# Kernel tuning notes

Hardware: AMD Instinct MI355X
Metric: run time of the kernel (lower is better)

## Reference

```python
import jax, jax.numpy as jnp
import numpy as np

N, M, E = 100000, 500, 300000
XS, GS, OUT, HEADS = 100, 100, 100, 2
SLOPE = 0.2
EPS = 1e-12


def l2norm(x, axis):
    n = jnp.linalg.norm(x, axis=axis, keepdims=True)
    return x / jnp.maximum(n, EPS)


def gat_layer(h_ijk, ends, n, W, att):
    # W: [heads*out, in_dim] (no bias); att: [1, heads, out]
    heads, out = att.shape[1], att.shape[2]
    c = (h_ijk @ W.T).reshape(-1, heads, out)               # [E, H, D]
    a = jnp.sum(att * c, axis=2, keepdims=True)             # [E, H, 1]
    e = jnp.exp(-jax.nn.leaky_relu(a, SLOPE))
    denom = jax.ops.segment_sum(e, ends, num_segments=n)    # [n, H, 1]
    alpha = e / denom[ends]                                 # segment softmax (dropout=eval/identity)
    h = jax.ops.segment_sum(alpha * c, ends, num_segments=n)  # [n, H, D]
    h = jax.nn.elu(h)
    h = l2norm(h, axis=2)
    return h.reshape(n, heads * out)


def merge_layer(h_in, h_out, Wi, bi, Wo, bo, Wl, bl):
    hi = h_in @ Wi.T + bi
    ho = h_out @ Wo.T + bo
    lam = jax.nn.sigmoid(jnp.concatenate([hi, ho], axis=1) @ Wl.T + bl)
    h = lam * hi + (1.0 - lam) * ho
    return l2norm(jax.nn.elu(h), axis=1)


def setup_inputs() -> dict:
    key = jax.random.key(0)
    ks = jax.random.split(key, 24)
    D = HEADS * OUT  # 200
    in1 = 2 * XS + GS   # 300
    in2 = 3 * D         # 600
    s = 0.05
    return {
        'edge_idx': jax.random.randint(ks[0], (2, E), 0, N),
        'edge_type': jax.random.randint(ks[1], (E,), 0, M),
        'path_idx': jax.random.randint(ks[2], (2, 8), 0, N),
        'path_type': jax.random.randint(ks[3], (2, 8), 0, M),
        'use_path': 0,
        'x': jax.random.normal(ks[4], (N, XS), jnp.float32),
        'g': jax.random.normal(ks[5], (M, GS), jnp.float32),
        'W_in1': s * jax.random.normal(ks[6], (D, in1), jnp.float32),
        'att_in1': s * jax.random.normal(ks[7], (1, HEADS, OUT), jnp.float32),
        'W_out1': s * jax.random.normal(ks[8], (D, in1), jnp.float32),
        'att_out1': s * jax.random.normal(ks[9], (1, HEADS, OUT), jnp.float32),
        'Wi1': s * jax.random.normal(ks[10], (D, D), jnp.float32), 'bi1': jnp.zeros((D,), jnp.float32),
        'Wo1': s * jax.random.normal(ks[11], (D, D), jnp.float32), 'bo1': jnp.zeros((D,), jnp.float32),
        'Wl1': s * jax.random.normal(ks[12], (1, 2 * D), jnp.float32), 'bl1': jnp.zeros((1,), jnp.float32),
        'Wr': s * jax.random.normal(ks[13], (D, GS), jnp.float32), 'br': jnp.zeros((D,), jnp.float32),
        'Wf': s * jax.random.normal(ks[14], (D, in1), jnp.float32), 'bf': jnp.zeros((D,), jnp.float32),
        'W_in2': s * jax.random.normal(ks[15], (D, in2), jnp.float32),
        'att_in2': s * jax.random.normal(ks[16], (1, 1, D), jnp.float32),
        'W_out2': s * jax.random.normal(ks[17], (D, in2), jnp.float32),
        'att_out2': s * jax.random.normal(ks[18], (1, 1, D), jnp.float32),
        'Wi2': s * jax.random.normal(ks[19], (D, D), jnp.float32), 'bi2': jnp.zeros((D,), jnp.float32),
        'Wo2': s * jax.random.normal(ks[20], (D, D), jnp.float32), 'bo2': jnp.zeros((D,), jnp.float32),
        'Wl2': s * jax.random.normal(ks[21], (1, 2 * D), jnp.float32), 'bl2': jnp.zeros((1,), jnp.float32),
        'W_ent': s * jax.random.normal(ks[22], (D, XS), jnp.float32),
    }


def reference(edge_idx, edge_type, path_idx, path_type, use_path, x, g,
              W_in1, att_in1, W_out1, att_out1, Wi1, bi1, Wo1, bo1, Wl1, bl1,
              Wr, br, Wf, bf,
              W_in2, att_in2, W_out2, att_out2, Wi2, bi2, Wo2, bo2, Wl2, bl2,
              W_ent):
    n, m = x.shape[0], g.shape[0]
    x = l2norm(x, axis=1)  # x_initial is renormalized each forward
    row, col = edge_idx[0], edge_idx[1]
    # hop 1: gather-concat per-edge features [E, 2*XS+GS]
    h_ijk = jnp.concatenate([x[row], x[col], g[edge_type]], axis=1)
    h_in = gat_layer(h_ijk, col, n, W_in1, att_in1)
    h_out = gat_layer(h_ijk, row, n, W_out1, att_out1)
    h = merge_layer(h_in, h_out, Wi1, bi1, Wo1, bo1, Wl1, bl1)
    # relation layer
    g_edges = jax.ops.segment_sum(h_ijk, edge_type, num_segments=m)
    g_edges = jax.nn.elu(l2norm(g_edges, axis=1))
    g_prime = (g @ Wr.T + br) + (g_edges @ Wf.T + bf)
    # hop 2
    h_ijk2 = jnp.concatenate([h[row], h[col], g_prime[edge_type]], axis=1)
    h_in2 = gat_layer(h_ijk2, col, n, W_in2, att_in2)
    h_out2 = gat_layer(h_ijk2, row, n, W_out2, att_out2)
    h = merge_layer(h_in2, h_out2, Wi2, bi2, Wo2, bo2, Wl2, bl2)
    # entity residual layer
    h_prime = x @ W_ent.T + h
    return h_prime
```

## Files before the change

kernel.cpp:

```cpp
#include <hip/hip_runtime.h>
#include <cstddef>
#include <cstdint>

#define WSLOPE 0.2f
#define WEPS 1e-12f

typedef __attribute__((ext_vector_type(8))) short bf16x8;
typedef __attribute__((ext_vector_type(4))) float f32x4;

__device__ __forceinline__ float waveSum(float v) {
#pragma unroll
    for (int off = 32; off > 0; off >>= 1) v += __shfl_xor(v, off, 64);
    return v;
}
__device__ __forceinline__ float eluf(float v) { return v > 0.f ? v : expm1f(v); }
__device__ __forceinline__ short f2bf(float f) {
    union { float f; uint32_t u; } v; v.f = f;
    uint32_t r = v.u + 0x7FFF + ((v.u >> 16) & 1);
    return (short)(r >> 16);
}
__device__ __forceinline__ float bf2f(short s) {
    union { uint32_t u; float f; } v; v.u = ((uint32_t)(uint16_t)s) << 16;
    return v.f;
}

__global__ void k_invnorm(const float* __restrict__ x, float* __restrict__ invn, int N) {
    int wid = blockIdx.x * 4 + (threadIdx.x >> 6);
    int lane = threadIdx.x & 63;
    if (wid >= N) return;
    const float* p = x + (size_t)wid * 100;
    float a = p[lane];
    float ss = a * a;
    if (lane < 36) { float b = p[lane + 64]; ss += b * b; }
    ss = waveSum(ss);
    if (lane == 0) invn[wid] = 1.f / fmaxf(sqrtf(ss), WEPS);
}

__global__ void k_count(const int* __restrict__ keys, int* __restrict__ cnt, int n) {
    int i = blockIdx.x * 256 + threadIdx.x;
    if (i < n) atomicAdd(&cnt[keys[i]], 1);
}

#define SCAN_CHUNK 2048
__global__ void k_blocksum(const int* __restrict__ cnt, int* __restrict__ bsum, int n) {
    __shared__ int sh[256];
    int b = blockIdx.x, t = threadIdx.x;
    int base = b * SCAN_CHUNK;
    int s = 0;
    for (int i = t; i < SCAN_CHUNK; i += 256) { int idx = base + i; if (idx < n) s += cnt[idx]; }
    sh[t] = s; __syncthreads();
    for (int off = 128; off > 0; off >>= 1) { if (t < off) sh[t] += sh[t + off]; __syncthreads(); }
    if (t == 0) bsum[b] = sh[0];
}

__global__ void k_scanwrite(const int* __restrict__ cnt, const int* __restrict__ bsum,
                            int* __restrict__ offs, int* __restrict__ cur, int n, int nb) {
    __shared__ int sh[256];
    __shared__ int sbase;
    int b = blockIdx.x, t = threadIdx.x;
    if (t == 0) { int s = 0; for (int i = 0; i < b; ++i) s += bsum[i]; sbase = s; }
    __syncthreads();
    int base = b * SCAN_CHUNK;
    int loc[8]; int ts = 0;
#pragma unroll
    for (int i = 0; i < 8; ++i) { int idx = base + t * 8 + i; int v = (idx < n) ? cnt[idx] : 0; loc[i] = ts; ts += v; }
    sh[t] = ts; __syncthreads();
    for (int off = 1; off < 256; off <<= 1) {
        int v = (t >= off) ? sh[t - off] : 0;
        __syncthreads();
        sh[t] += v;
        __syncthreads();
    }
    int excl = (t == 0) ? 0 : sh[t - 1];
    int gbase = sbase + excl;
#pragma unroll
    for (int i = 0; i < 8; ++i) {
        int idx = base + t * 8 + i;
        if (idx < n) { offs[idx] = gbase + loc[i]; cur[idx] = gbase + loc[i]; }
    }
    if (b == nb - 1 && t == 255) offs[n] = sbase + sh[255];
}

__global__ void k_scatter3(const int* __restrict__ keys, const int* __restrict__ other,
                           const int* __restrict__ et, int* __restrict__ cur,
                           int* __restrict__ nbrS, int* __restrict__ etS,
                           int* __restrict__ keyS, int n) {
    int i = blockIdx.x * 256 + threadIdx.x;
    if (i < n) {
        int p = atomicAdd(&cur[keys[i]], 1);
        nbrS[p] = other[i];
        etS[p] = et[i];
        keyS[p] = keys[i];
    }
}

__global__ void k_scatter2(const int* __restrict__ keys, int* __restrict__ cur,
                           int* __restrict__ rs, int* __restrict__ cs,
                           const int* __restrict__ row, const int* __restrict__ col, int n) {
    int i = blockIdx.x * 256 + threadIdx.x;
    if (i < n) {
        int p = atomicAdd(&cur[keys[i]], 1);
        rs[p] = row[i];
        cs[p] = col[i];
    }
}

__global__ void k_watt(const float* __restrict__ att, const float* __restrict__ W,
                       float* __restrict__ wa, int H, int DH, int K) {
    int id = blockIdx.x * 256 + threadIdx.x;
    if (id >= H * K) return;
    int h = id / K, k = id % K;
    float s = 0.f;
    for (int j = 0; j < DH; ++j) s += att[h * DH + j] * W[(size_t)(h * DH + j) * K + k];
    wa[id] = s;
}

template<bool HOP2>
__global__ void k_dots(const float* __restrict__ feat, const float* __restrict__ invn,
                       const float* __restrict__ wa, float* __restrict__ rdot,
                       float* __restrict__ cdot, int N) {
    int wid = blockIdx.x * 4 + (threadIdx.x >> 6);
    int lane = threadIdx.x & 63;
    if (wid >= N) return;
    if (!HOP2) {
        float inv = invn[wid];
        const float* p = feat + (size_t)wid * 100;
        float f0 = p[lane] * inv;
        float f1 = (lane < 36) ? p[lane + 64] * inv : 0.f;
#pragma unroll
        for (int h = 0; h < 2; ++h) {
            const float* w = wa + h * 300;
            float r = f0 * w[lane] + ((lane < 36) ? f1 * w[lane + 64] : 0.f);
            float c = f0 * w[100 + lane] + ((lane < 36) ? f1 * w[100 + lane + 64] : 0.f);
            r = waveSum(r); c = waveSum(c);
            if (lane == 0) { rdot[wid * 2 + h] = r; cdot[wid * 2 + h] = c; }
        }
    } else {
        const float* p = feat + (size_t)wid * 200;
        float r = 0.f, c = 0.f;
#pragma unroll
        for (int m = 0; m < 4; ++m) {
            int d = lane + m * 64;
            if (d < 200) { float f = p[d]; r += f * wa[d]; c += f * wa[200 + d]; }
        }
        r = waveSum(r); c = waveSum(c);
        if (lane == 0) { rdot[wid] = r; cdot[wid] = c; }
    }
}

__global__ void k_gdot(const float* __restrict__ gsrc, const float* __restrict__ wa,
                       float* __restrict__ gdot, int M, int H, int GL, int K) {
    int id = blockIdx.x * 256 + threadIdx.x;
    if (id >= M * H) return;
    int m = id / H, h = id % H;
    float s = 0.f;
    const float* w = wa + h * K + 2 * GL;
    const float* gm = gsrc + (size_t)m * GL;
    for (int kk = 0; kk < GL; ++kk) s += gm[kk] * w[kk];
    gdot[id] = s;
}

__global__ void k_ew_s(const int* __restrict__ nbrS, const int* __restrict__ keyS,
                       const int* __restrict__ etS,
                       const float* __restrict__ ndot, const float* __restrict__ kdot,
                       const float* __restrict__ gdot, float* __restrict__ ewS, int E, int H) {
    int id = blockIdx.x * 256 + threadIdx.x;
    if (id >= E * H) return;
    int p = id / H, h = id - p * H;
    float a = ndot[nbrS[p] * H + h] + kdot[keyS[p] * H + h] + gdot[etS[p] * H + h];
    float lr = a > 0.f ? a : WSLOPE * a;
    ewS[id] = expf(-lr);
}

template<bool HOP2>
__global__ void k_agg(const int* __restrict__ offs, const int* __restrict__ nbrS,
                      const int* __restrict__ etS, const float* __restrict__ ewS,
                      const short* __restrict__ featB, const short* __restrict__ gB,
                      short* __restrict__ A, int n0, int n1) {
    constexpr int H = HOP2 ? 1 : 2;
    constexpr int LDA = HOP2 ? 672 : 576;
    constexpr int FW = HOP2 ? 224 : 112;
    constexpr int GW = HOP2 ? 224 : 112;
    int node = n0 + blockIdx.x * 4 + (threadIdx.x >> 6);
    int lane = threadIdx.x & 63;
    if (node >= n1) return;
    int o = offs[node];
    int deg = offs[node + 1] - o;
    float va[7];
#pragma unroll
    for (int m = 0; m < 7; ++m) va[m] = 0.f;
    if (deg > 0) {
        float s0 = 0.f, s1 = 0.f;
        for (int i = lane; i < deg; i += 64) {
            s0 += ewS[(size_t)(o + i) * H];
            if (H == 2) s1 += ewS[(size_t)(o + i) * H + 1];
        }
        s0 = waveSum(s0);
        float rd0 = 1.f / s0, rd1 = rd0;
        if (H == 2) { s1 = waveSum(s1); rd1 = 1.f / s1; }
        for (int j = 0; j < deg; ++j) {
            float a0 = ewS[(size_t)(o + j) * H] * rd0;
            float a1 = (H == 2) ? ewS[(size_t)(o + j) * H + 1] * rd1 : a0;
            int nbr = nbrS[o + j];
            int et = etS[o + j];
            const short* fr = featB + (size_t)nbr * FW;
            const short* gr = gB + (size_t)et * GW;
            if (!HOP2) {
#pragma unroll
                for (int m = 0; m < 7; ++m) {
                    int d = lane + m * 64;
                    if (d < 100) va[m] += a0 * bf2f(fr[d]);
                    else if (d < 200) va[m] += a1 * bf2f(fr[d - 100]);
                    else if (d < 300) va[m] += a0 * bf2f(gr[d - 200]);
                    else if (d < 400) va[m] += a1 * bf2f(gr[d - 300]);
                }
            } else {
#pragma unroll
                for (int m = 0; m < 7; ++m) {
                    int d = lane + m * 64;
                    if (d < 200) va[m] += a0 * bf2f(fr[d]);
                    else if (d < 424) va[m] += a0 * bf2f(gr[d - 200]);
                }
            }
        }
    }
    size_t rb = (size_t)(node - n0);
    short* Ar = A + rb * LDA;
    if (!HOP2) {
#pragma unroll
        for (int m = 0; m < 7; ++m) {
            int d = lane + m * 64;
            if (d < 400) {
                int col = d < 100 ? d : (d < 200 ? d + 12 : (d < 300 ? d + 24 : d + 36));
                Ar[col] = f2bf(va[m]);
            }
        }
        if (lane < 48) { int q = lane / 12; int rm = lane - q * 12; Ar[q * 112 + 100 + rm] = 0; }
        const short* sf = featB + (size_t)node * 112;
#pragma unroll
        for (int mm = 0; mm < 2; ++mm) {
            int k = lane + mm * 64;
            if (k < 128) Ar[448 + k] = (deg > 0 && k < 112) ? sf[k] : (short)0;
        }
    } else {
#pragma unroll
        for (int m = 0; m < 7; ++m) {
            int d = lane + m * 64;
            if (d < 424) Ar[d < 200 ? d : d + 24] = f2bf(va[m]);
        }
        if (lane < 24) Ar[200 + lane] = 0;
        const short* sf = featB + (size_t)node * 224;
#pragma unroll
        for (int mm = 0; mm < 4; ++mm) {
            int k = lane + mm * 64;
            if (k < 224) Ar[448 + k] = deg > 0 ? sf[k] : (short)0;
        }
    }
}

template<int KSTEPS, bool BIAS, bool ACC>
__launch_bounds__(256)
__global__ void k_mgemm(const short* __restrict__ A, const short* __restrict__ Wb,
                        const float* __restrict__ bias,
                        float* __restrict__ out, int rows, int lda) {
    constexpr int LDW = KSTEPS * 32;
    const int t = threadIdx.x;
    const int wv = t >> 6, l = t & 63;
    const int lhi = l >> 4, llo = l & 15;
    const int rbase = blockIdx.x * 64 + wv * 16;
    f32x4 acc[13];
#pragma unroll
    for (int j = 0; j < 13; ++j) acc[j] = f32x4{0.f, 0.f, 0.f, 0.f};
    const short* arow = A + (size_t)(rbase + llo) * lda + lhi * 8;
#pragma unroll
    for (int kt = 0; kt < KSTEPS; ++kt) {
        bf16x8 a = *(const bf16x8*)(arow + kt * 32);
#pragma unroll
        for (int j = 0; j < 13; ++j) {
            bf16x8 b = *(const bf16x8*)(Wb + (size_t)(j * 16 + llo) * LDW + kt * 32 + lhi * 8);
            acc[j] = __builtin_amdgcn_mfma_f32_16x16x32_bf16(a, b, acc[j], 0, 0, 0);
        }
    }
    const int r0 = rbase + lhi * 4;
#pragma unroll
    for (int e = 0; e < 4; ++e) {
        int r = r0 + e;
        if (r >= rows) continue;
        float* orow = out + (size_t)r * 200;
#pragma unroll
        for (int j = 0; j < 13; ++j) {
            int d = j * 16 + llo;
            if (d < 200) {
                float v = acc[j][e];
                if (BIAS) v += bias[d];
                if (ACC) v += orow[d];
                orow[d] = v;
            }
        }
    }
}

__global__ void k_prepw(const float* __restrict__ W, int ldW, int koff, int Klen, int span,
                        int mode, short* __restrict__ Wb, int ldWb, int dst) {
    int id = blockIdx.x * 256 + threadIdx.x;
    int tot = 208 * span;
    if (id >= tot) return;
    int d = id / span, k = id - d * span;
    float v = 0.f;
    if (d < 200) {
        if (mode == 0) { if (k < Klen) v = W[(size_t)d * ldW + koff + k]; }
        else { int h = d / 100; int kk = k - h * 112; if (kk >= 0 && kk < Klen) v = W[(size_t)d * ldW + koff + kk]; }
    }
    Wb[(size_t)d * ldWb + dst + k] = f2bf(v);
}

__global__ void k_prepwrf(const float* __restrict__ Wr, const float* __restrict__ Wf,
                          short* __restrict__ Wb) {
    int id = blockIdx.x * 256 + threadIdx.x;
    if (id >= 208 * 448) return;
    int d = id / 448, k = id - d * 448;
    float v = 0.f;
    if (d < 200) {
        if (k < 100) v = Wr[(size_t)d * 100 + k];
        else if (k >= 128 && k < 428) v = Wf[(size_t)d * 300 + (k - 128)];
    }
    Wb[id] = f2bf(v);
}

__global__ void k_brf(const float* __restrict__ br, const float* __restrict__ bf,
                      float* __restrict__ brf) {
    int d = threadIdx.x;
    if (d < 200) brf[d] = br[d] + bf[d];
}

__global__ void k_cvt112(const float* __restrict__ src, const float* __restrict__ invn,
                         short* __restrict__ dst, int rows) {
    int id = blockIdx.x * 256 + threadIdx.x;
    if (id >= rows * 112) return;
    int r = id / 112, k = id - r * 112;
    float v = 0.f;
    if (k < 100) { v = src[(size_t)r * 100 + k]; if (invn) v *= invn[r]; }
    dst[id] = f2bf(v);
}

__global__ void k_gcb(const float* __restrict__ g, short* __restrict__ gb, int rows) {
    int id = blockIdx.x * 256 + threadIdx.x;
    if (id >= rows * 128) return;
    int r = id >> 7, k = id & 127;
    gb[(size_t)r * 448 + k] = f2bf(k < 100 ? g[(size_t)r * 100 + k] : 0.f);
}

__global__ void k_h1b(const float* __restrict__ h1, short* __restrict__ sb, int rows) {
    int id = blockIdx.x * 256 + threadIdx.x;
    if (id >= rows * 224) return;
    int r = id / 224, k = id - r * 224;
    sb[id] = f2bf(k < 200 ? h1[(size_t)r * 200 + k] : 0.f);
}

template<int DH, int H>
__global__ void gat_post2(const float* __restrict__ hb, short* __restrict__ pb, int rowsH) {
    int nh = blockIdx.x * 4 + (threadIdx.x >> 6);
    int lane = threadIdx.x & 63;
    if (nh >= rowsH) return;
    const float* p = hb + (size_t)nh * DH;
    constexpr int MM = (DH + 63) / 64;
    float v[MM];
    float ss = 0.f;
#pragma unroll
    for (int m = 0; m < MM; ++m) {
        int d = lane + m * 64;
        v[m] = 0.f;
        if (d < DH) { v[m] = eluf(p[d]); ss += v[m] * v[m]; }
    }
    ss = waveSum(ss);
    float inv = 1.f / fmaxf(sqrtf(ss), WEPS);
    short* ob = pb + (size_t)(nh / H) * 224 + (size_t)(nh % H) * DH;
#pragma unroll
    for (int m = 0; m < MM; ++m) {
        int d = lane + m * 64;
        if (d < DH) ob[d] = f2bf(v[m] * inv);
    }
}

__global__ void merge_comb(const float* __restrict__ hi, const float* __restrict__ ho,
                           const float* __restrict__ Wl, const float* __restrict__ bl,
                           float* __restrict__ out, short* __restrict__ hbf, int N) {
    int wid = blockIdx.x * 4 + (threadIdx.x >> 6);
    int lane = threadIdx.x & 63;
    if (wid >= N) return;
    float vi[4], vo[4];
    float s = 0.f;
#pragma unroll
    for (int m = 0; m < 4; ++m) {
        int d = lane + m * 64;
        vi[m] = 0.f; vo[m] = 0.f;
        if (d < 200) {
            vi[m] = hi[(size_t)wid * 200 + d];
            vo[m] = ho[(size_t)wid * 200 + d];
            s += Wl[d] * vi[m] + Wl[200 + d] * vo[m];
        }
    }
    s = waveSum(s);
    float lam = 1.f / (1.f + expf(-(s + bl[0])));
    float hv[4];
    float ss = 0.f;
#pragma unroll
    for (int m = 0; m < 4; ++m) {
        int d = lane + m * 64;
        hv[m] = 0.f;
        if (d < 200) {
            float h = lam * vi[m] + (1.f - lam) * vo[m];
            hv[m] = eluf(h);
            ss += hv[m] * hv[m];
        }
    }
    ss = waveSum(ss);
    float inv = 1.f / fmaxf(sqrtf(ss), WEPS);
#pragma unroll
    for (int m = 0; m < 4; ++m) {
        int d = lane + m * 64;
        if (d < 200) {
            float v = hv[m] * inv;
            out[(size_t)wid * 200 + d] = v;
            if (hbf) hbf[(size_t)wid * 224 + d] = f2bf(v);
        } else if (d < 224) {
            if (hbf) hbf[(size_t)wid * 224 + d] = 0;
        }
    }
}

__global__ void k_gedges_b(const int* __restrict__ rsT, const int* __restrict__ csT,
                           const int* __restrict__ offsT,
                           const float* __restrict__ x, const float* __restrict__ invn,
                           const float* __restrict__ g, short* __restrict__ gcomb, int M) {
    __shared__ float red[6];
    int m = blockIdx.x, t = threadIdx.x;
    int o = offsT[m];
    int deg = offsT[m + 1] - o;
    float acc = 0.f;
    if (t < 128) {
        int d = t; bool ok = d < 100;
        for (int i = 0; i < deg; ++i) {
            int r = rsT[o + i];
            if (ok) acc += x[(size_t)r * 100 + d] * invn[r];
        }
    } else if (t < 256) {
        int d = t - 128; bool ok = d < 100;
        for (int i = 0; i < deg; ++i) {
            int c = csT[o + i];
            if (ok) acc += x[(size_t)c * 100 + d] * invn[c];
        }
    } else {
        int d = t - 256;
        if (d < 100) acc = (float)deg * g[(size_t)m * 100 + d];
    }
    float sq = waveSum(acc * acc);
    if ((t & 63) == 0) red[t >> 6] = sq;
    __syncthreads();
    float s2 = red[0] + red[1] + red[2] + red[3] + red[4] + red[5];
    float inv = 1.f / fmaxf(sqrtf(s2), WEPS);
    short* orow = gcomb + (size_t)m * 448 + 128;
    if (t < 128) {
        if (t < 100) orow[t] = f2bf(eluf(acc * inv));
    } else if (t < 256) {
        int d = t - 128;
        if (d < 100) orow[100 + d] = f2bf(eluf(acc * inv));
    } else {
        int d = t - 256;
        if (d < 100) orow[200 + d] = f2bf(eluf(acc * inv));
        else if (d < 120) orow[200 + d] = 0;
    }
}

extern "C" void kernel_launch(void* const* d_in, const int* in_sizes, int n_in,
                              void* d_out, int out_size, void* d_ws, size_t ws_size,
                              hipStream_t stream) {
    const int* eidx   = (const int*)d_in[0];
    const int* etype  = (const int*)d_in[1];
    const float* x    = (const float*)d_in[5];
    const float* g    = (const float*)d_in[6];
    const float* W_in1  = (const float*)d_in[7];
    const float* att_in1 = (const float*)d_in[8];
    const float* W_out1 = (const float*)d_in[9];
    const float* att_out1 = (const float*)d_in[10];
    const float* Wi1 = (const float*)d_in[11]; const float* bi1 = (const float*)d_in[12];
    const float* Wo1 = (const float*)d_in[13]; const float* bo1 = (const float*)d_in[14];
    const float* Wl1 = (const float*)d_in[15]; const float* bl1 = (const float*)d_in[16];
    const float* Wr  = (const float*)d_in[17]; const float* br  = (const float*)d_in[18];
    const float* Wf  = (const float*)d_in[19]; const float* bf  = (const float*)d_in[20];
    const float* W_in2  = (const float*)d_in[21]; const float* att_in2 = (const float*)d_in[22];
    const float* W_out2 = (const float*)d_in[23]; const float* att_out2 = (const float*)d_in[24];
    const float* Wi2 = (const float*)d_in[25]; const float* bi2 = (const float*)d_in[26];
    const float* Wo2 = (const float*)d_in[27]; const float* bo2 = (const float*)d_in[28];
    const float* Wl2 = (const float*)d_in[29]; const float* bl2 = (const float*)d_in[30];
    const float* W_ent = (const float*)d_in[31];

    const int E = in_sizes[1];
    const int N = in_sizes[5] / 100;
    const int M = in_sizes[6] / 100;
    const int Mr = (M + 63) & ~63;
    float* out = (float*)d_out;
    const int* row = eidx;
    const int* col = eidx + E;

    char* w = (char*)d_ws;
    size_t off_b = 0;
    auto alloc = [&](size_t bytes) -> void* {
        void* p = w + off_b;
        off_b += (bytes + 255) & ~(size_t)255;
        return p;
    };
    float* invn  = (float*)alloc((size_t)N * 4);
    float* h1    = (float*)alloc((size_t)N * 200 * 4);
    short* h1_bf = (short*)alloc((size_t)(N + 64) * 224 * 2);
    short* xn_bf = (short*)alloc((size_t)(N + 64) * 112 * 2);
    short* g_bf  = (short*)alloc((size_t)M * 112 * 2);
    int* offs_in = (int*)alloc((size_t)(N + 1) * 4);
    int* offs_out= (int*)alloc((size_t)(N + 1) * 4);
    int* offsT   = (int*)alloc((size_t)(M + 1) * 4);
    int* nbrS_in = (int*)alloc((size_t)E * 4);
    int* etS_in  = (int*)alloc((size_t)E * 4);
    int* keyS_in = (int*)alloc((size_t)E * 4);
    int* nbrS_out= (int*)alloc((size_t)E * 4);
    int* etS_out = (int*)alloc((size_t)E * 4);
    int* keyS_out= (int*)alloc((size_t)E * 4);
    int* rsT     = (int*)alloc((size_t)E * 4);
    int* csT     = (int*)alloc((size_t)E * 4);
    int* cnt     = (int*)alloc((size_t)N * 4);
    int* cur     = (int*)alloc((size_t)N * 4);
    int* bsum    = (int*)alloc((size_t)64 * 4);
    float* wa_in = (float*)alloc((size_t)1200 * 4);
    float* wa_out= (float*)alloc((size_t)1200 * 4);
    float* rdot_in = (float*)alloc((size_t)N * 2 * 4);
    float* cdot_in = (float*)alloc((size_t)N * 2 * 4);
    float* rdot_out= (float*)alloc((size_t)N * 2 * 4);
    float* cdot_out= (float*)alloc((size_t)N * 2 * 4);
    float* gdot_in = (float*)alloc((size_t)M * 2 * 4);
    float* gdot_out= (float*)alloc((size_t)M * 2 * 4);
    float* ewS_in  = (float*)alloc((size_t)E * 2 * 4);
    float* ewS_out = (float*)alloc((size_t)E * 2 * 4);
    float* gp      = (float*)alloc((size_t)M * 200 * 4);
    short* gcomb   = (short*)alloc((size_t)Mr * 448 * 2);
    short* Wc_in1  = (short*)alloc((size_t)208 * 576 * 2);
    short* Wc_out1 = (short*)alloc((size_t)208 * 576 * 2);
    short* Wc_in2  = (short*)alloc((size_t)208 * 672 * 2);
    short* Wc_out2 = (short*)alloc((size_t)208 * 672 * 2);
    short* Wm_i1   = (short*)alloc((size_t)208 * 224 * 2);
    short* Wm_o1   = (short*)alloc((size_t)208 * 224 * 2);
    short* Wm_i2   = (short*)alloc((size_t)208 * 224 * 2);
    short* Wm_o2   = (short*)alloc((size_t)208 * 224 * 2);
    short* Wb_ent  = (short*)alloc((size_t)208 * 128 * 2);
    short* Wrf_b   = (short*)alloc((size_t)208 * 448 * 2);
    float* brf     = (float*)alloc((size_t)200 * 4);

    if (off_b >= ws_size) return;
    size_t rem = ws_size - off_b;
    long long Cll = (long long)(rem / 3520);
    long long Nr64 = ((long long)N + 63) & ~63LL;
    int C = (int)(Cll > Nr64 ? Nr64 : Cll);
    C &= ~63;
    if (C < 64) return;
    float* hbA   = (float*)alloc((size_t)C * 200 * 4);
    float* hbB   = (float*)alloc((size_t)C * 200 * 4);
    short* Ac    = (short*)alloc((size_t)C * 672 * 2);
    short* post_b= (short*)alloc((size_t)C * 224 * 2);
    if (off_b > ws_size) return;

    const int gE = (E + 255) / 256;
    const int gN4 = (N + 3) / 4;
    const int gM64 = (M + 63) / 64;

    k_invnorm<<<gN4, 256, 0, stream>>>(x, invn, N);

    hipMemsetAsync(post_b, 0, (size_t)C * 224 * 2, stream);

    k_cvt112<<<((int)(((size_t)N * 112 + 255) / 256)), 256, 0, stream>>>(x, invn, xn_bf, N);
    k_cvt112<<<((int)(((size_t)M * 112 + 255) / 256)), 256, 0, stream>>>(g, nullptr, g_bf, M);

    auto gsp = [](int span) { return (208 * span + 255) / 256; };
    k_prepw<<<gsp(224), 256, 0, stream>>>(W_in1, 300, 0, 100, 224, 1, Wc_in1, 576, 0);
    k_prepw<<<gsp(224), 256, 0, stream>>>(W_in1, 300, 200, 100, 224, 1, Wc_in1, 576, 224);
    k_prepw<<<gsp(128), 256, 0, stream>>>(W_in1, 300, 100, 100, 128, 0, Wc_in1, 576, 448);
    k_prepw<<<gsp(224), 256, 0, stream>>>(W_out1, 300, 100, 100, 224, 1, Wc_out1, 576, 0);
    k_prepw<<<gsp(224), 256, 0, stream>>>(W_out1, 300, 200, 100, 224, 1, Wc_out1, 576, 224);
    k_prepw<<<gsp(128), 256, 0, stream>>>(W_out1, 300, 0, 100, 128, 0, Wc_out1, 576, 448);
    k_prepw<<<gsp(224), 256, 0, stream>>>(W_in2, 600, 0, 200, 224, 0, Wc_in2, 672, 0);
    k_prepw<<<gsp(224), 256, 0, stream>>>(W_in2, 600, 400, 200, 224, 0, Wc_in2, 672, 224);
    k_prepw<<<gsp(224), 256, 0, stream>>>(W_in2, 600, 200, 200, 224, 0, Wc_in2, 672, 448);
    k_prepw<<<gsp(224), 256, 0, stream>>>(W_out2, 600, 200, 200, 224, 0, Wc_out2, 672, 0);
    k_prepw<<<gsp(224), 256, 0, stream>>>(W_out2, 600, 400, 200, 224, 0, Wc_out2, 672, 224);
    k_prepw<<<gsp(224), 256, 0, stream>>>(W_out2, 600, 0, 200, 224, 0, Wc_out2, 672, 448);
    k_prepw<<<gsp(224), 256, 0, stream>>>(Wi1, 200, 0, 200, 224, 0, Wm_i1, 224, 0);
    k_prepw<<<gsp(224), 256, 0, stream>>>(Wo1, 200, 0, 200, 224, 0, Wm_o1, 224, 0);
    k_prepw<<<gsp(224), 256, 0, stream>>>(Wi2, 200, 0, 200, 224, 0, Wm_i2, 224, 0);
    k_prepw<<<gsp(224), 256, 0, stream>>>(Wo2, 200, 0, 200, 224, 0, Wm_o2, 224, 0);
    k_prepw<<<gsp(128), 256, 0, stream>>>(W_ent, 100, 0, 100, 128, 0, Wb_ent, 128, 0);
    k_prepwrf<<<gsp(448), 256, 0, stream>>>(Wr, Wf, Wrf_b);
    k_brf<<<1, 256, 0, stream>>>(br, bf, brf);

    int nbN = (N + SCAN_CHUNK - 1) / SCAN_CHUNK;
    int nbM = (M + SCAN_CHUNK - 1) / SCAN_CHUNK;
    hipMemsetAsync(cnt, 0, (size_t)N * 4, stream);
    k_count<<<gE, 256, 0, stream>>>(col, cnt, E);
    k_blocksum<<<nbN, 256, 0, stream>>>(cnt, bsum, N);
    k_scanwrite<<<nbN, 256, 0, stream>>>(cnt, bsum, offs_in, cur, N, nbN);
    k_scatter3<<<gE, 256, 0, stream>>>(col, row, etype, cur, nbrS_in, etS_in, keyS_in, E);

    hipMemsetAsync(cnt, 0, (size_t)N * 4, stream);
    k_count<<<gE, 256, 0, stream>>>(row, cnt, E);
    k_blocksum<<<nbN, 256, 0, stream>>>(cnt, bsum, N);
    k_scanwrite<<<nbN, 256, 0, stream>>>(cnt, bsum, offs_out, cur, N, nbN);
    k_scatter3<<<gE, 256, 0, stream>>>(row, col, etype, cur, nbrS_out, etS_out, keyS_out, E);

    hipMemsetAsync(cnt, 0, (size_t)M * 4, stream);
    k_count<<<gE, 256, 0, stream>>>(etype, cnt, E);
    k_blocksum<<<nbM, 256, 0, stream>>>(cnt, bsum, M);
    k_scanwrite<<<nbM, 256, 0, stream>>>(cnt, bsum, offsT, cur, M, nbM);
    k_scatter2<<<gE, 256, 0, stream>>>(etype, cur, rsT, csT, row, col, E);

    k_watt<<<(2 * 300 + 255) / 256, 256, 0, stream>>>(att_in1, W_in1, wa_in, 2, 100, 300);
    k_watt<<<(2 * 300 + 255) / 256, 256, 0, stream>>>(att_out1, W_out1, wa_out, 2, 100, 300);
    k_dots<false><<<gN4, 256, 0, stream>>>(x, invn, wa_in, rdot_in, cdot_in, N);
    k_dots<false><<<gN4, 256, 0, stream>>>(x, invn, wa_out, rdot_out, cdot_out, N);
    k_gdot<<<(M * 2 + 255) / 256, 256, 0, stream>>>(g, wa_in, gdot_in, M, 2, 100, 300);
    k_gdot<<<(M * 2 + 255) / 256, 256, 0, stream>>>(g, wa_out, gdot_out, M, 2, 100, 300);
    k_ew_s<<<(E * 2 + 255) / 256, 256, 0, stream>>>(nbrS_in, keyS_in, etS_in, rdot_in, cdot_in, gdot_in, ewS_in, E, 2);
    k_ew_s<<<(E * 2 + 255) / 256, 256, 0, stream>>>(nbrS_out, keyS_out, etS_out, cdot_out, rdot_out, gdot_out, ewS_out, E, 2);
    k_gcb<<<((int)(((size_t)M * 128 + 255) / 256)), 256, 0, stream>>>(g, gcomb, M);

    for (int n0 = 0; n0 < N; n0 += C) {
        int rows = (N - n0 < C) ? (N - n0) : C;
        int n1 = n0 + rows;
        int ga = (rows + 3) / 4;
        int gb = (rows + 63) / 64;
        k_agg<false><<<ga, 256, 0, stream>>>(offs_in, nbrS_in, etS_in, ewS_in, xn_bf, g_bf, Ac, n0, n1);
        k_mgemm<18, false, false><<<gb, 256, 0, stream>>>(Ac, Wc_in1, nullptr, hbA, rows, 576);
        gat_post2<100, 2><<<(2 * rows + 3) / 4, 256, 0, stream>>>(hbA, post_b, 2 * rows);
        k_mgemm<7, true, false><<<gb, 256, 0, stream>>>(post_b, Wm_i1, bi1, hbA, rows, 224);
        k_agg<false><<<ga, 256, 0, stream>>>(offs_out, nbrS_out, etS_out, ewS_out, xn_bf, g_bf, Ac, n0, n1);
        k_mgemm<18, false, false><<<gb, 256, 0, stream>>>(Ac, Wc_out1, nullptr, hbB, rows, 576);
        gat_post2<100, 2><<<(2 * rows + 3) / 4, 256, 0, stream>>>(hbB, post_b, 2 * rows);
        k_mgemm<7, true, false><<<gb, 256, 0, stream>>>(post_b, Wm_o1, bo1, hbB, rows, 224);
        merge_comb<<<ga, 256, 0, stream>>>(hbA, hbB, Wl1, bl1, h1 + (size_t)n0 * 200,
                                           h1_bf + (size_t)n0 * 224, rows);
    }

    k_gedges_b<<<M, 384, 0, stream>>>(rsT, csT, offsT, x, invn, g, gcomb, M);
    k_mgemm<14, true, false><<<gM64, 256, 0, stream>>>(gcomb, Wrf_b, brf, gp, M, 448);

    k_watt<<<(600 + 255) / 256, 256, 0, stream>>>(att_in2, W_in2, wa_in, 1, 200, 600);
    k_watt<<<(600 + 255) / 256, 256, 0, stream>>>(att_out2, W_out2, wa_out, 1, 200, 600);
    k_dots<true><<<gN4, 256, 0, stream>>>(h1, nullptr, wa_in, rdot_in, cdot_in, N);
    k_dots<true><<<gN4, 256, 0, stream>>>(h1, nullptr, wa_out, rdot_out, cdot_out, N);
    k_gdot<<<(M + 255) / 256, 256, 0, stream>>>(gp, wa_in, gdot_in, M, 1, 200, 600);
    k_gdot<<<(M + 255) / 256, 256, 0, stream>>>(gp, wa_out, gdot_out, M, 1, 200, 600);
    k_h1b<<<((int)(((size_t)M * 224 + 255) / 256)), 256, 0, stream>>>(gp, gcomb, M);
    k_ew_s<<<(E + 255) / 256, 256, 0, stream>>>(nbrS_in, keyS_in, etS_in, rdot_in, cdot_in, gdot_in, ewS_in, E, 1);
    k_ew_s<<<(E + 255) / 256, 256, 0, stream>>>(nbrS_out, keyS_out, etS_out, cdot_out, rdot_out, gdot_out, ewS_out, E, 1);

    for (int n0 = 0; n0 < N; n0 += C) {
        int rows = (N - n0 < C) ? (N - n0) : C;
        int n1 = n0 + rows;
        int ga = (rows + 3) / 4;
        int gb = (rows + 63) / 64;
        k_agg<true><<<ga, 256, 0, stream>>>(offs_in, nbrS_in, etS_in, ewS_in, h1_bf, gcomb, Ac, n0, n1);
        k_mgemm<21, false, false><<<gb, 256, 0, stream>>>(Ac, Wc_in2, nullptr, hbA, rows, 672);
        gat_post2<200, 1><<<ga, 256, 0, stream>>>(hbA, post_b, rows);
        k_mgemm<7, true, false><<<gb, 256, 0, stream>>>(post_b, Wm_i2, bi2, hbA, rows, 224);
        k_agg<true><<<ga, 256, 0, stream>>>(offs_out, nbrS_out, etS_out, ewS_out, h1_bf, gcomb, Ac, n0, n1);
        k_mgemm<21, false, false><<<gb, 256, 0, stream>>>(Ac, Wc_out2, nullptr, hbB, rows, 672);
        gat_post2<200, 1><<<ga, 256, 0, stream>>>(hbB, post_b, rows);
        k_mgemm<7, true, false><<<gb, 256, 0, stream>>>(post_b, Wm_o2, bo2, hbB, rows, 224);
        merge_comb<<<ga, 256, 0, stream>>>(hbA, hbB, Wl2, bl2, out + (size_t)n0 * 200, nullptr, rows);
        k_mgemm<4, false, true><<<gb, 256, 0, stream>>>(xn_bf + (size_t)n0 * 112, Wb_ent, nullptr,
                                                        out + (size_t)n0 * 200, rows, 112);
    }
}
```

Before: 2.887 ms.

## Fuse GAT epilogues, merge layer and hop-2 attention dots into MFMA GEMM kernels

The ELU+L2-norm post-processing now runs in the GEMM epilogue, and the two merge projections plus the sigmoid gate, ELU and norm run in one dual-GEMM kernel. Hop-2 attention dot products come from that same epilogue, and relation-layer g' dots come from its GEMM epilogue. This drops the fp32 intermediate buffers (h1, hbA/hbB, gp), several separate launches and the kernels that reread those buffers. It frees workspace for larger chunks, at the cost of higher register pressure in the fused kernels and 16-lane shuffle reductions.

```diff
diff --git a/kernel.cpp b/kernel.cpp
--- a/kernel.cpp
+++ b/kernel.cpp
@@ -11,6 +11,11 @@
 __device__ __forceinline__ float waveSum(float v) {
 #pragma unroll
     for (int off = 32; off > 0; off >>= 1) v += __shfl_xor(v, off, 64);
+    return v;
+}
+__device__ __forceinline__ float rowSum16(float v) {
+#pragma unroll
+    for (int off = 8; off > 0; off >>= 1) v += __shfl_xor(v, off, 64);
     return v;
 }
 __device__ __forceinline__ float eluf(float v) { return v > 0.f ? v : expm1f(v); }
@@ -115,49 +120,44 @@
     wa[id] = s;
 }
 
-template<bool HOP2>
-__global__ void k_dots(const float* __restrict__ feat, const float* __restrict__ invn,
-                       const float* __restrict__ wa, float* __restrict__ rdot,
-                       float* __restrict__ cdot, int N) {
+__global__ void k_dots2(const float* __restrict__ x, const float* __restrict__ invn,
+                        const float* __restrict__ wai, const float* __restrict__ wao,
+                        float* __restrict__ rdi, float* __restrict__ cdi,
+                        float* __restrict__ rdo, float* __restrict__ cdo, int N) {
     int wid = blockIdx.x * 4 + (threadIdx.x >> 6);
     int lane = threadIdx.x & 63;
     if (wid >= N) return;
-    if (!HOP2) {
-        float inv = invn[wid];
-        const float* p = feat + (size_t)wid * 100;
-        float f0 = p[lane] * inv;
-        float f1 = (lane < 36) ? p[lane + 64] * inv : 0.f;
-#pragma unroll
-        for (int h = 0; h < 2; ++h) {
-            const float* w = wa + h * 300;
-            float r = f0 * w[lane] + ((lane < 36) ? f1 * w[lane + 64] : 0.f);
-            float c = f0 * w[100 + lane] + ((lane < 36) ? f1 * w[100 + lane + 64] : 0.f);
-            r = waveSum(r); c = waveSum(c);
-            if (lane == 0) { rdot[wid * 2 + h] = r; cdot[wid * 2 + h] = c; }
-        }
-    } else {
-        const float* p = feat + (size_t)wid * 200;
-        float r = 0.f, c = 0.f;
-#pragma unroll
-        for (int m = 0; m < 4; ++m) {
-            int d = lane + m * 64;
-            if (d < 200) { float f = p[d]; r += f * wa[d]; c += f * wa[200 + d]; }
-        }
-        r = waveSum(r); c = waveSum(c);
-        if (lane == 0) { rdot[wid] = r; cdot[wid] = c; }
-    }
-}
-
-__global__ void k_gdot(const float* __restrict__ gsrc, const float* __restrict__ wa,
-                       float* __restrict__ gdot, int M, int H, int GL, int K) {
-    int id = blockIdx.x * 256 + threadIdx.x;
-    if (id >= M * H) return;
-    int m = id / H, h = id % H;
-    float s = 0.f;
-    const float* w = wa + h * K + 2 * GL;
-    const float* gm = gsrc + (size_t)m * GL;
-    for (int kk = 0; kk < GL; ++kk) s += gm[kk] * w[kk];
-    gdot[id] = s;
+    float inv = invn[wid];
+    const float* p = x + (size_t)wid * 100;
+    float f0 = p[lane] * inv;
+    float f1 = (lane < 36) ? p[lane + 64] * inv : 0.f;
+#pragma unroll
+    for (int h = 0; h < 2; ++h) {
+        const float* wi = wai + h * 300;
+        const float* wo = wao + h * 300;
+        float ri = f0 * wi[lane] + ((lane < 36) ? f1 * wi[lane + 64] : 0.f);
+        float ci = f0 * wi[100 + lane] + ((lane < 36) ? f1 * wi[100 + lane + 64] : 0.f);
+        float ro = f0 * wo[lane] + ((lane < 36) ? f1 * wo[lane + 64] : 0.f);
+        float co = f0 * wo[100 + lane] + ((lane < 36) ? f1 * wo[100 + lane + 64] : 0.f);
+        ri = waveSum(ri); ci = waveSum(ci); ro = waveSum(ro); co = waveSum(co);
+        if (lane == 0) { rdi[wid * 2 + h] = ri; cdi[wid * 2 + h] = ci; rdo[wid * 2 + h] = ro; cdo[wid * 2 + h] = co; }
+    }
+}
+
+__global__ void k_gdot4(const float* __restrict__ g, const float* __restrict__ wai,
+                        const float* __restrict__ wao, float* __restrict__ gdi,
+                        float* __restrict__ gdo, int M) {
+    int m = blockIdx.x * 256 + threadIdx.x;
+    if (m >= M) return;
+    const float* gm = g + (size_t)m * 100;
+    float s0 = 0.f, s1 = 0.f, s2 = 0.f, s3 = 0.f;
+    for (int k = 0; k < 100; ++k) {
+        float v = gm[k];
+        s0 += v * wai[200 + k]; s1 += v * wai[500 + k];
+        s2 += v * wao[200 + k]; s3 += v * wao[500 + k];
+    }
+    gdi[m * 2] = s0; gdi[m * 2 + 1] = s1;
+    gdo[m * 2] = s2; gdo[m * 2 + 1] = s3;
 }
 
 __global__ void k_ew_s(const int* __restrict__ nbrS, const int* __restrict__ keyS,
@@ -300,6 +300,191 @@
     }
 }
 
+template<int KSTEPS, int H>
+__launch_bounds__(256)
+__global__ void k_mgemm_post(const short* __restrict__ A, const short* __restrict__ Wb,
+                             short* __restrict__ post, int rows, int lda) {
+    constexpr int LDW = KSTEPS * 32;
+    const int t = threadIdx.x;
+    const int wv = t >> 6, l = t & 63;
+    const int lhi = l >> 4, llo = l & 15;
+    const int rbase = blockIdx.x * 64 + wv * 16;
+    f32x4 acc[13];
+#pragma unroll
+    for (int j = 0; j < 13; ++j) acc[j] = f32x4{0.f, 0.f, 0.f, 0.f};
+    const short* arow = A + (size_t)(rbase + llo) * lda + lhi * 8;
+#pragma unroll
+    for (int kt = 0; kt < KSTEPS; ++kt) {
+        bf16x8 a = *(const bf16x8*)(arow + kt * 32);
+#pragma unroll
+        for (int j = 0; j < 13; ++j) {
+            bf16x8 b = *(const bf16x8*)(Wb + (size_t)(j * 16 + llo) * LDW + kt * 32 + lhi * 8);
+            acc[j] = __builtin_amdgcn_mfma_f32_16x16x32_bf16(a, b, acc[j], 0, 0, 0);
+        }
+    }
+    const int r0 = rbase + lhi * 4;
+#pragma unroll
+    for (int e = 0; e < 4; ++e) {
+        int r = r0 + e;
+        if (r >= rows) continue;
+        float v[13];
+        float s0 = 0.f, s1 = 0.f;
+#pragma unroll
+        for (int j = 0; j < 13; ++j) {
+            int d = j * 16 + llo;
+            if (d < 200) {
+                float xv = eluf(acc[j][e]);
+                v[j] = xv;
+                if (H == 1 || d < 100) s0 += xv * xv; else s1 += xv * xv;
+            }
+        }
+        s0 = rowSum16(s0);
+        float inv0 = 1.f / fmaxf(sqrtf(s0), WEPS);
+        float inv1 = inv0;
+        if (H == 2) { s1 = rowSum16(s1); inv1 = 1.f / fmaxf(sqrtf(s1), WEPS); }
+        short* pr = post + (size_t)r * 224;
+#pragma unroll
+        for (int j = 0; j < 13; ++j) {
+            int d = j * 16 + llo;
+            if (d < 200) pr[d] = f2bf(v[j] * ((H == 2 && d >= 100) ? inv1 : inv0));
+        }
+    }
+}
+
+template<bool HOP1>
+__launch_bounds__(256)
+__global__ void k_mergemm(const short* __restrict__ pA, const short* __restrict__ pB,
+                          const short* __restrict__ Wi, const short* __restrict__ Wo,
+                          const float* __restrict__ bi, const float* __restrict__ bo,
+                          const float* __restrict__ Wl, const float* __restrict__ bl,
+                          float* __restrict__ outf, short* __restrict__ h1b,
+                          const float* __restrict__ wa2i, const float* __restrict__ wa2o,
+                          float* __restrict__ rdi, float* __restrict__ cdi,
+                          float* __restrict__ rdo, float* __restrict__ cdo,
+                          int rows) {
+    const int t = threadIdx.x;
+    const int wv = t >> 6, l = t & 63;
+    const int lhi = l >> 4, llo = l & 15;
+    const int rbase = blockIdx.x * 64 + wv * 16;
+    f32x4 accA[13], accB[13];
+#pragma unroll
+    for (int j = 0; j < 13; ++j) { accA[j] = f32x4{0.f, 0.f, 0.f, 0.f}; accB[j] = f32x4{0.f, 0.f, 0.f, 0.f}; }
+    const short* aA = pA + (size_t)(rbase + llo) * 224 + lhi * 8;
+    const short* aB = pB + (size_t)(rbase + llo) * 224 + lhi * 8;
+#pragma unroll
+    for (int kt = 0; kt < 7; ++kt) {
+        bf16x8 a1 = *(const bf16x8*)(aA + kt * 32);
+        bf16x8 a2 = *(const bf16x8*)(aB + kt * 32);
+#pragma unroll
+        for (int j = 0; j < 13; ++j) {
+            bf16x8 b1 = *(const bf16x8*)(Wi + (size_t)(j * 16 + llo) * 224 + kt * 32 + lhi * 8);
+            accA[j] = __builtin_amdgcn_mfma_f32_16x16x32_bf16(a1, b1, accA[j], 0, 0, 0);
+            bf16x8 b2 = *(const bf16x8*)(Wo + (size_t)(j * 16 + llo) * 224 + kt * 32 + lhi * 8);
+            accB[j] = __builtin_amdgcn_mfma_f32_16x16x32_bf16(a2, b2, accB[j], 0, 0, 0);
+        }
+    }
+    const int r0 = rbase + lhi * 4;
+    float blv = bl[0];
+#pragma unroll
+    for (int e = 0; e < 4; ++e) {
+        int r = r0 + e;
+        if (r >= rows) continue;
+        float vi[13], vo[13];
+        float lp = 0.f;
+#pragma unroll
+        for (int j = 0; j < 13; ++j) {
+            int d = j * 16 + llo;
+            if (d < 200) {
+                vi[j] = accA[j][e] + bi[d];
+                vo[j] = accB[j][e] + bo[d];
+                lp += Wl[d] * vi[j] + Wl[200 + d] * vo[j];
+            }
+        }
+        lp = rowSum16(lp);
+        float lam = 1.f / (1.f + expf(-(lp + blv)));
+        float hv[13];
+        float ss = 0.f;
+#pragma unroll
+        for (int j = 0; j < 13; ++j) {
+            int d = j * 16 + llo;
+            if (d < 200) { hv[j] = eluf(lam * vi[j] + (1.f - lam) * vo[j]); ss += hv[j] * hv[j]; }
+        }
+        ss = rowSum16(ss);
+        float inv = 1.f / fmaxf(sqrtf(ss), WEPS);
+        float ri = 0.f, ci = 0.f, ro = 0.f, co = 0.f;
+#pragma unroll
+        for (int j = 0; j < 13; ++j) {
+            int d = j * 16 + llo;
+            if (d < 200) {
+                float val = hv[j] * inv;
+                if (HOP1) {
+                    h1b[(size_t)r * 224 + d] = f2bf(val);
+                    ri += val * wa2i[d]; ci += val * wa2i[200 + d];
+                    ro += val * wa2o[d]; co += val * wa2o[200 + d];
+                } else {
+                    outf[(size_t)r * 200 + d] = val;
+                }
+            } else if (HOP1) {
+                h1b[(size_t)r * 224 + d] = 0;
+            }
+        }
+        if (HOP1) {
+            h1b[(size_t)r * 224 + 208 + llo] = 0;
+            ri = rowSum16(ri); ci = rowSum16(ci); ro = rowSum16(ro); co = rowSum16(co);
+            if (llo == 0) { rdi[r] = ri; cdi[r] = ci; rdo[r] = ro; cdo[r] = co; }
+        }
+    }
+}
+
+__launch_bounds__(256)
+__global__ void k_mgemm_rel(const short* __restrict__ A, const short* __restrict__ Wb,
+                            const float* __restrict__ brf,
+                            short* __restrict__ gout, const float* __restrict__ wai,
+                            const float* __restrict__ wao,
+                            float* __restrict__ gdi, float* __restrict__ gdo, int rows) {
+    constexpr int KSTEPS = 14, LDW = KSTEPS * 32;
+    const int t = threadIdx.x;
+    const int wv = t >> 6, l = t & 63;
+    const int lhi = l >> 4, llo = l & 15;
+    const int rbase = blockIdx.x * 64 + wv * 16;
+    f32x4 acc[13];
+#pragma unroll
+    for (int j = 0; j < 13; ++j) acc[j] = f32x4{0.f, 0.f, 0.f, 0.f};
+    const short* arow = A + (size_t)(rbase + llo) * 448 + lhi * 8;
+#pragma unroll
+    for (int kt = 0; kt < KSTEPS; ++kt) {
+        bf16x8 a = *(const bf16x8*)(arow + kt * 32);
+#pragma unroll
+        for (int j = 0; j < 13; ++j) {
+            bf16x8 b = *(const bf16x8*)(Wb + (size_t)(j * 16 + llo) * LDW + kt * 32 + lhi * 8);
+            acc[j] = __builtin_amdgcn_mfma_f32_16x16x32_bf16(a, b, acc[j], 0, 0, 0);
+        }
+    }
+    const int r0 = rbase + lhi * 4;
+#pragma unroll
+    for (int e = 0; e < 4; ++e) {
+        int r = r0 + e;
+        if (r >= rows) continue;
+        short* pr = gout + (size_t)r * 224;
+        float gi = 0.f, go = 0.f;
+#pragma unroll
+        for (int j = 0; j < 13; ++j) {
+            int d = j * 16 + llo;
+            if (d < 200) {
+                float val = acc[j][e] + brf[d];
+                pr[d] = f2bf(val);
+                gi += val * wai[400 + d];
+                go += val * wao[400 + d];
+            } else {
+                pr[d] = 0;
+            }
+        }
+        pr[208 + llo] = 0;
+        gi = rowSum16(gi); go = rowSum16(go);
+        if (llo == 0) { gdi[r] = gi; gdo[r] = go; }
+    }
+}
+
 __global__ void k_prepw(const float* __restrict__ W, int ldW, int koff, int Klen, int span,
                         int mode, short* __restrict__ Wb, int ldWb, int dst) {
     int id = blockIdx.x * 256 + threadIdx.x;
@@ -348,85 +533,6 @@
     if (id >= rows * 128) return;
     int r = id >> 7, k = id & 127;
     gb[(size_t)r * 448 + k] = f2bf(k < 100 ? g[(size_t)r * 100 + k] : 0.f);
-}
-
-__global__ void k_h1b(const float* __restrict__ h1, short* __restrict__ sb, int rows) {
-    int id = blockIdx.x * 256 + threadIdx.x;
-    if (id >= rows * 224) return;
-    int r = id / 224, k = id - r * 224;
-    sb[id] = f2bf(k < 200 ? h1[(size_t)r * 200 + k] : 0.f);
-}
-
-template<int DH, int H>
-__global__ void gat_post2(const float* __restrict__ hb, short* __restrict__ pb, int rowsH) {
-    int nh = blockIdx.x * 4 + (threadIdx.x >> 6);
-    int lane = threadIdx.x & 63;
-    if (nh >= rowsH) return;
-    const float* p = hb + (size_t)nh * DH;
-    constexpr int MM = (DH + 63) / 64;
-    float v[MM];
-    float ss = 0.f;
-#pragma unroll
-    for (int m = 0; m < MM; ++m) {
-        int d = lane + m * 64;
-        v[m] = 0.f;
-        if (d < DH) { v[m] = eluf(p[d]); ss += v[m] * v[m]; }
-    }
-    ss = waveSum(ss);
-    float inv = 1.f / fmaxf(sqrtf(ss), WEPS);
-    short* ob = pb + (size_t)(nh / H) * 224 + (size_t)(nh % H) * DH;
-#pragma unroll
-    for (int m = 0; m < MM; ++m) {
-        int d = lane + m * 64;
-        if (d < DH) ob[d] = f2bf(v[m] * inv);
-    }
-}
-
-__global__ void merge_comb(const float* __restrict__ hi, const float* __restrict__ ho,
-                           const float* __restrict__ Wl, const float* __restrict__ bl,
-                           float* __restrict__ out, short* __restrict__ hbf, int N) {
-    int wid = blockIdx.x * 4 + (threadIdx.x >> 6);
-    int lane = threadIdx.x & 63;
-    if (wid >= N) return;
-    float vi[4], vo[4];
-    float s = 0.f;
-#pragma unroll
-    for (int m = 0; m < 4; ++m) {
-        int d = lane + m * 64;
-        vi[m] = 0.f; vo[m] = 0.f;
-        if (d < 200) {
-            vi[m] = hi[(size_t)wid * 200 + d];
-            vo[m] = ho[(size_t)wid * 200 + d];
-            s += Wl[d] * vi[m] + Wl[200 + d] * vo[m];
-        }
-    }
-    s = waveSum(s);
-    float lam = 1.f / (1.f + expf(-(s + bl[0])));
-    float hv[4];
-    float ss = 0.f;
-#pragma unroll
-    for (int m = 0; m < 4; ++m) {
-        int d = lane + m * 64;
-        hv[m] = 0.f;
-        if (d < 200) {
-            float h = lam * vi[m] + (1.f - lam) * vo[m];
-            hv[m] = eluf(h);
-            ss += hv[m] * hv[m];
-        }
-    }
-    ss = waveSum(ss);
-    float inv = 1.f / fmaxf(sqrtf(ss), WEPS);
-#pragma unroll
-    for (int m = 0; m < 4; ++m) {
-        int d = lane + m * 64;
-        if (d < 200) {
-            float v = hv[m] * inv;
-            out[(size_t)wid * 200 + d] = v;
-            if (hbf) hbf[(size_t)wid * 224 + d] = f2bf(v);
-        } else if (d < 224) {
-            if (hbf) hbf[(size_t)wid * 224 + d] = 0;
-        }
-    }
 }
 
 __global__ void k_gedges_b(const int* __restrict__ rsT, const int* __restrict__ csT,
@@ -511,10 +617,10 @@
         return p;
     };
     float* invn  = (float*)alloc((size_t)N * 4);
-    float* h1    = (float*)alloc((size_t)N * 200 * 4);
     short* h1_bf = (short*)alloc((size_t)(N + 64) * 224 * 2);
     short* xn_bf = (short*)alloc((size_t)(N + 64) * 112 * 2);
     short* g_bf  = (short*)alloc((size_t)M * 112 * 2);
+    short* gp_bf = (short*)alloc((size_t)Mr * 224 * 2);
     int* offs_in = (int*)alloc((size_t)(N + 1) * 4);
     int* offs_out= (int*)alloc((size_t)(N + 1) * 4);
     int* offsT   = (int*)alloc((size_t)(M + 1) * 4);
@@ -529,8 +635,10 @@
     int* cnt     = (int*)alloc((size_t)N * 4);
     int* cur     = (int*)alloc((size_t)N * 4);
     int* bsum    = (int*)alloc((size_t)64 * 4);
-    float* wa_in = (float*)alloc((size_t)1200 * 4);
-    float* wa_out= (float*)alloc((size_t)1200 * 4);
+    float* wa1_in = (float*)alloc((size_t)640 * 4);
+    float* wa1_out= (float*)alloc((size_t)640 * 4);
+    float* wa2_in = (float*)alloc((size_t)640 * 4);
+    float* wa2_out= (float*)alloc((size_t)640 * 4);
     float* rdot_in = (float*)alloc((size_t)N * 2 * 4);
     float* cdot_in = (float*)alloc((size_t)N * 2 * 4);
     float* rdot_out= (float*)alloc((size_t)N * 2 * 4);
@@ -539,7 +647,6 @@
     float* gdot_out= (float*)alloc((size_t)M * 2 * 4);
     float* ewS_in  = (float*)alloc((size_t)E * 2 * 4);
     float* ewS_out = (float*)alloc((size_t)E * 2 * 4);
-    float* gp      = (float*)alloc((size_t)M * 200 * 4);
     short* gcomb   = (short*)alloc((size_t)Mr * 448 * 2);
     short* Wc_in1  = (short*)alloc((size_t)208 * 576 * 2);
     short* Wc_out1 = (short*)alloc((size_t)208 * 576 * 2);
@@ -555,15 +662,14 @@
 
     if (off_b >= ws_size) return;
     size_t rem = ws_size - off_b;
-    long long Cll = (long long)(rem / 3520);
+    long long Cll = (long long)(rem / 2368);
     long long Nr64 = ((long long)N + 63) & ~63LL;
     int C = (int)(Cll > Nr64 ? Nr64 : Cll);
     C &= ~63;
     if (C < 64) return;
-    float* hbA   = (float*)alloc((size_t)C * 200 * 4);
-    float* hbB   = (float*)alloc((size_t)C * 200 * 4);
     short* Ac    = (short*)alloc((size_t)C * 672 * 2);
-    short* post_b= (short*)alloc((size_t)C * 224 * 2);
+    short* postA = (short*)alloc((size_t)C * 224 * 2);
+    short* postB = (short*)alloc((size_t)C * 224 * 2);
     if (off_b > ws_size) return;
 
     const int gE = (E + 255) / 256;
@@ -572,7 +678,8 @@
 
     k_invnorm<<<gN4, 256, 0, stream>>>(x, invn, N);
 
-    hipMemsetAsync(post_b, 0, (size_t)C * 224 * 2, stream);
+    hipMemsetAsync(postA, 0, (size_t)C * 224 * 2, stream);
+    hipMemsetAsync(postB, 0, (size_t)C * 224 * 2, stream);
 
     k_cvt112<<<((int)(((size_t)N * 112 + 255) / 256)), 256, 0, stream>>>(x, invn, xn_bf, N);
     k_cvt112<<<((int)(((size_t)M * 112 + 255) / 256)), 256, 0, stream>>>(g, nullptr, g_bf, M);
@@ -618,12 +725,13 @@
     k_scanwrite<<<nbM, 256, 0, stream>>>(cnt, bsum, offsT, cur, M, nbM);
     k_scatter2<<<gE, 256, 0, stream>>>(etype, cur, rsT, csT, row, col, E);
 
-    k_watt<<<(2 * 300 + 255) / 256, 256, 0, stream>>>(att_in1, W_in1, wa_in, 2, 100, 300);
-    k_watt<<<(2 * 300 + 255) / 256, 256, 0, stream>>>(att_out1, W_out1, wa_out, 2, 100, 300);
-    k_dots<false><<<gN4, 256, 0, stream>>>(x, invn, wa_in, rdot_in, cdot_in, N);
-    k_dots<false><<<gN4, 256, 0, stream>>>(x, invn, wa_out, rdot_out, cdot_out, N);
-    k_gdot<<<(M * 2 + 255) / 256, 256, 0, stream>>>(g, wa_in, gdot_in, M, 2, 100, 300);
-    k_gdot<<<(M * 2 + 255) / 256, 256, 0, stream>>>(g, wa_out, gdot_out, M, 2, 100, 300);
+    k_watt<<<(600 + 255) / 256, 256, 0, stream>>>(att_in1, W_in1, wa1_in, 2, 100, 300);
+    k_watt<<<(600 + 255) / 256, 256, 0, stream>>>(att_out1, W_out1, wa1_out, 2, 100, 300);
+    k_watt<<<(600 + 255) / 256, 256, 0, stream>>>(att_in2, W_in2, wa2_in, 1, 200, 600);
+    k_watt<<<(600 + 255) / 256, 256, 0, stream>>>(att_out2, W_out2, wa2_out, 1, 200, 600);
+
+    k_dots2<<<gN4, 256, 0, stream>>>(x, invn, wa1_in, wa1_out, rdot_in, cdot_in, rdot_out, cdot_out, N);
+    k_gdot4<<<(M + 255) / 256, 256, 0, stream>>>(g, wa1_in, wa1_out, gdot_in, gdot_out, M);
     k_ew_s<<<(E * 2 + 255) / 256, 256, 0, stream>>>(nbrS_in, keyS_in, etS_in, rdot_in, cdot_in, gdot_in, ewS_in, E, 2);
     k_ew_s<<<(E * 2 + 255) / 256, 256, 0, stream>>>(nbrS_out, keyS_out, etS_out, cdot_out, rdot_out, gdot_out, ewS_out, E, 2);
     k_gcb<<<((int)(((size_t)M * 128 + 255) / 256)), 256, 0, stream>>>(g, gcomb, M);
@@ -634,27 +742,18 @@
         int ga = (rows + 3) / 4;
         int gb = (rows + 63) / 64;
         k_agg<false><<<ga, 256, 0, stream>>>(offs_in, nbrS_in, etS_in, ewS_in, xn_bf, g_bf, Ac, n0, n1);
-        k_mgemm<18, false, false><<<gb, 256, 0, stream>>>(Ac, Wc_in1, nullptr, hbA, rows, 576);
-        gat_post2<100, 2><<<(2 * rows + 3) / 4, 256, 0, stream>>>(hbA, post_b, 2 * rows);
-        k_mgemm<7, true, false><<<gb, 256, 0, stream>>>(post_b, Wm_i1, bi1, hbA, rows, 224);
+        k_mgemm_post<18, 2><<<gb, 256, 0, stream>>>(Ac, Wc_in1, postA, rows, 576);
         k_agg<false><<<ga, 256, 0, stream>>>(offs_out, nbrS_out, etS_out, ewS_out, xn_bf, g_bf, Ac, n0, n1);
-        k_mgemm<18, false, false><<<gb, 256, 0, stream>>>(Ac, Wc_out1, nullptr, hbB, rows, 576);
-        gat_post2<100, 2><<<(2 * rows + 3) / 4, 256, 0, stream>>>(hbB, post_b, 2 * rows);
-        k_mgemm<7, true, false><<<gb, 256, 0, stream>>>(post_b, Wm_o1, bo1, hbB, rows, 224);
-        merge_comb<<<ga, 256, 0, stream>>>(hbA, hbB, Wl1, bl1, h1 + (size_t)n0 * 200,
-                                           h1_bf + (size_t)n0 * 224, rows);
+        k_mgemm_post<18, 2><<<gb, 256, 0, stream>>>(Ac, Wc_out1, postB, rows, 576);
+        k_mergemm<true><<<gb, 256, 0, stream>>>(postA, postB, Wm_i1, Wm_o1, bi1, bo1, Wl1, bl1,
+                                                nullptr, h1_bf + (size_t)n0 * 224, wa2_in, wa2_out,
+                                                rdot_in + n0, cdot_in + n0, rdot_out + n0, cdot_out + n0,
+                                                rows);
     }
 
     k_gedges_b<<<M, 384, 0, stream>>>(rsT, csT, offsT, x, invn, g, gcomb, M);
-    k_mgemm<14, true, false><<<gM64, 256, 0, stream>>>(gcomb, Wrf_b, brf, gp, M, 448);
-
-    k_watt<<<(600 + 255) / 256, 256, 0, stream>>>(att_in2, W_in2, wa_in, 1, 200, 600);
-    k_watt<<<(600 + 255) / 256, 256, 0, stream>>>(att_out2, W_out2, wa_out, 1, 200, 600);
-    k_dots<true><<<gN4, 256, 0, stream>>>(h1, nullptr, wa_in, rdot_in, cdot_in, N);
-    k_dots<true><<<gN4, 256, 0, stream>>>(h1, nullptr, wa_out, rdot_out, cdot_out, N);
-    k_gdot<<<(M + 255) / 256, 256, 0, stream>>>(gp, wa_in, gdot_in, M, 1, 200, 600);
-    k_gdot<<<(M + 255) / 256, 256, 0, stream>>>(gp, wa_out, gdot_out, M, 1, 200, 600);
-    k_h1b<<<((int)(((size_t)M * 224 + 255) / 256)), 256, 0, stream>>>(gp, gcomb, M);
+    k_mgemm_rel<<<gM64, 256, 0, stream>>>(gcomb, Wrf_b, brf, gp_bf, wa2_in, wa2_out, gdot_in, gdot_out, M);
+
     k_ew_s<<<(E + 255) / 256, 256, 0, stream>>>(nbrS_in, keyS_in, etS_in, rdot_in, cdot_in, gdot_in, ewS_in, E, 1);
     k_ew_s<<<(E + 255) / 256, 256, 0, stream>>>(nbrS_out, keyS_out, etS_out, cdot_out, rdot_out, gdot_out, ewS_out, E, 1);
 
@@ -663,15 +762,13 @@
         int n1 = n0 + rows;
         int ga = (rows + 3) / 4;
         int gb = (rows + 63) / 64;
-        k_agg<true><<<ga, 256, 0, stream>>>(offs_in, nbrS_in, etS_in, ewS_in, h1_bf, gcomb, Ac, n0, n1);
-        k_mgemm<21, false, false><<<gb, 256, 0, stream>>>(Ac, Wc_in2, nullptr, hbA, rows, 672);
-        gat_post2<200, 1><<<ga, 256, 0, stream>>>(hbA, post_b, rows);
-        k_mgemm<7, true, false><<<gb, 256, 0, stream>>>(post_b, Wm_i2, bi2, hbA, rows, 224);
-        k_agg<true><<<ga, 256, 0, stream>>>(offs_out, nbrS_out, etS_out, ewS_out, h1_bf, gcomb, Ac, n0, n1);
-        k_mgemm<21, false, false><<<gb, 256, 0, stream>>>(Ac, Wc_out2, nullptr, hbB, rows, 672);
-        gat_post2<200, 1><<<ga, 256, 0, stream>>>(hbB, post_b, rows);
-        k_mgemm<7, true, false><<<gb, 256, 0, stream>>>(post_b, Wm_o2, bo2, hbB, rows, 224);
-        merge_comb<<<ga, 256, 0, stream>>>(hbA, hbB, Wl2, bl2, out + (size_t)n0 * 200, nullptr, rows);
+        k_agg<true><<<ga, 256, 0, stream>>>(offs_in, nbrS_in, etS_in, ewS_in, h1_bf, gp_bf, Ac, n0, n1);
+        k_mgemm_post<21, 1><<<gb, 256, 0, stream>>>(Ac, Wc_in2, postA, rows, 672);
+        k_agg<true><<<ga, 256, 0, stream>>>(offs_out, nbrS_out, etS_out, ewS_out, h1_bf, gp_bf, Ac, n0, n1);
+        k_mgemm_post<21, 1><<<gb, 256, 0, stream>>>(Ac, Wc_out2, postB, rows, 672);
+        k_mergemm<false><<<gb, 256, 0, stream>>>(postA, postB, Wm_i2, Wm_o2, bi2, bo2, Wl2, bl2,
+                                                 out + (size_t)n0 * 200, nullptr, nullptr, nullptr,
+                                                 nullptr, nullptr, nullptr, nullptr, rows);
         k_mgemm<4, false, true><<<gb, 256, 0, stream>>>(xn_bf + (size_t)n0 * 112, Wb_ent, nullptr,
                                                         out + (size_t)n0 * 200, rows, 112);
     }
```

New measurement: 2.859 ms. Within noise of the previous version (-1.0%).
